# Kernel optimization log

Hardware: AMD Instinct MI355X
Metric: run time of the kernel (lower is better)

Reference implementation:

```python
import jax, jax.numpy as jnp
import numpy as np


def setup_inputs() -> dict:
    key = jax.random.key(0)
    k1, k2 = jax.random.split(key)
    x = jax.random.normal(k1, (4096, 8192), dtype=jnp.float32)
    idx = jax.random.randint(k2, (4096, 8192), 0, 1000000, dtype=jnp.int32)
    return {"input": x, "indices": idx}


def reference(input, indices):
    # elementwise: sin where index even, cos where index odd
    even = (indices % 2) == 0
    return jnp.where(even, jnp.sin(input), jnp.cos(input))
```

## Files before the change

kernel.cpp:

```cpp
#include <hip/hip_runtime.h>


__global__ void __launch_bounds__(256) sincos_sel_kernel(
    const float4* __restrict__ x,
    const int4*  __restrict__ idx,
    float4* __restrict__ out,
    int n4)
{
    const int stride = gridDim.x * blockDim.x;
    for (int i = blockIdx.x * blockDim.x + threadIdx.x; i < n4; i += stride) {
        float4 xv = x[i];
        int4   iv = idx[i];
        float4 o;
        o.x = (iv.x & 1) ? __cosf(xv.x) : __sinf(xv.x);
        o.y = (iv.y & 1) ? __cosf(xv.y) : __sinf(xv.y);
        o.z = (iv.z & 1) ? __cosf(xv.z) : __sinf(xv.z);
        o.w = (iv.w & 1) ? __cosf(xv.w) : __sinf(xv.w);
        out[i] = o;
    }
}

extern "C" void kernel_launch(void* const* d_in, const int* in_sizes, int n_in,
                              void* d_out, int out_size, void* d_ws, size_t ws_size,
                              hipStream_t stream)
{
    const float* x   = (const float*)d_in[0];
    const int*   idx = (const int*)d_in[1];
    float*       out = (float*)d_out;

    const int n  = in_sizes[0];
    const int n4 = n >> 2;

    const int block = 256;
    const int grid  = 2048;

    sincos_sel_kernel<<<grid, block, 0, stream>>>(
        (const float4*)x, (const int4*)idx, (float4*)out, n4);
}
```

Before: 80.09 us.

## Unroll grid-stride loop 4x, use hardware sin with phase shift, nontemporal stores

Each thread now issues four independent 16-byte loads per array before computing, which raises memory-level parallelism. Sine and cosine become a single hardware v_sin on the argument scaled by 1/(2π), with a quarter-period offset for odd indices, so the select branch disappears. Outputs use nontemporal stores to avoid polluting cache. Accuracy depends on the hardware sin's range handling for large arguments. Inputs here are standard normal, so they stay small.

Measured after the change: 66.19 us. -17.4%, faster.

```diff
diff --git a/kernel.cpp b/kernel.cpp
--- a/kernel.cpp
+++ b/kernel.cpp
@@ -1,22 +1,55 @@
 #include <hip/hip_runtime.h>
 
 
+typedef float vfloat4 __attribute__((ext_vector_type(4)));
+typedef int   vint4   __attribute__((ext_vector_type(4)));
+
+__device__ __forceinline__ float sincos_sel(float x, int odd) {
+    const float INV2PI = 0.15915493667125702f;
+    float t = __builtin_fmaf(x, INV2PI, odd ? 0.25f : 0.0f);
+    return __builtin_amdgcn_sinf(t);
+}
+
 __global__ void __launch_bounds__(256) sincos_sel_kernel(
-    const float4* __restrict__ x,
-    const int4*  __restrict__ idx,
-    float4* __restrict__ out,
+    const vfloat4* __restrict__ x,
+    const vint4*  __restrict__ idx,
+    vfloat4* __restrict__ out,
     int n4)
 {
+    const int tid    = blockIdx.x * blockDim.x + threadIdx.x;
     const int stride = gridDim.x * blockDim.x;
-    for (int i = blockIdx.x * blockDim.x + threadIdx.x; i < n4; i += stride) {
-        float4 xv = x[i];
-        int4   iv = idx[i];
-        float4 o;
-        o.x = (iv.x & 1) ? __cosf(xv.x) : __sinf(xv.x);
-        o.y = (iv.y & 1) ? __cosf(xv.y) : __sinf(xv.y);
-        o.z = (iv.z & 1) ? __cosf(xv.z) : __sinf(xv.z);
-        o.w = (iv.w & 1) ? __cosf(xv.w) : __sinf(xv.w);
-        out[i] = o;
+
+    int i = tid;
+    for (; i + 3 * stride < n4; i += 4 * stride) {
+        vfloat4 x0 = x[i];
+        vfloat4 x1 = x[i +     stride];
+        vfloat4 x2 = x[i + 2 * stride];
+        vfloat4 x3 = x[i + 3 * stride];
+        vint4   d0 = idx[i];
+        vint4   d1 = idx[i +     stride];
+        vint4   d2 = idx[i + 2 * stride];
+        vint4   d3 = idx[i + 3 * stride];
+
+        vfloat4 o0, o1, o2, o3;
+        #pragma unroll
+        for (int j = 0; j < 4; ++j) {
+            o0[j] = sincos_sel(x0[j], d0[j] & 1);
+            o1[j] = sincos_sel(x1[j], d1[j] & 1);
+            o2[j] = sincos_sel(x2[j], d2[j] & 1);
+            o3[j] = sincos_sel(x3[j], d3[j] & 1);
+        }
+        __builtin_nontemporal_store(o0, &out[i]);
+        __builtin_nontemporal_store(o1, &out[i +     stride]);
+        __builtin_nontemporal_store(o2, &out[i + 2 * stride]);
+        __builtin_nontemporal_store(o3, &out[i + 3 * stride]);
+    }
+    for (; i < n4; i += stride) {
+        vfloat4 xv = x[i];
+        vint4   dv = idx[i];
+        vfloat4 o;
+        #pragma unroll
+        for (int j = 0; j < 4; ++j) o[j] = sincos_sel(xv[j], dv[j] & 1);
+        __builtin_nontemporal_store(o, &out[i]);
     }
 }
 
@@ -24,9 +57,9 @@
                               void* d_out, int out_size, void* d_ws, size_t ws_size,
                               hipStream_t stream)
 {
-    const float* x   = (const float*)d_in[0];
-    const int*   idx = (const int*)d_in[1];
-    float*       out = (float*)d_out;
+    const vfloat4* x   = (const vfloat4*)d_in[0];
+    const vint4*   idx = (const vint4*)d_in[1];
+    vfloat4*       out = (vfloat4*)d_out;
 
     const int n  = in_sizes[0];
     const int n4 = n >> 2;
@@ -34,6 +67,5 @@
     const int block = 256;
     const int grid  = 2048;
 
-    sincos_sel_kernel<<<grid, block, 0, stream>>>(
-        (const float4*)x, (const int4*)idx, (float4*)out, n4);
+    sincos_sel_kernel<<<grid, block, 0, stream>>>(x, idx, out, n4);
 }
```
